# Performance work log

Measured on AMD Instinct MI355X. Metric: run time of the kernel, lower is better.

Reference implementation:

```python
import jax, jax.numpy as jnp
import numpy as np

B, P, K = 8, 1024, 20  # clouds, points per cloud, kNN neighbors
OUT = 40
EPS = 1e-5


def leaky(x):
    return jnp.where(x >= 0, x, 0.2 * x)


def batch_norm(h, gamma, beta):
    mu = jnp.mean(h, axis=0)
    var = jnp.var(h, axis=0)
    return (h - mu) * jax.lax.rsqrt(var + EPS) * gamma + beta


def edge_conv(x, W, b, k):
    # x: [B,P,C]. Dynamic kNN in feature space (self included, as torch_cluster knn),
    # edge feature nn([x_i, x_j - x_i]) (single plain Linear per PyG MLP plain_last),
    # then max-aggregation over the k neighbors.
    sq = jnp.sum(x * x, axis=-1)                                  # [B,P]
    d = sq[:, :, None] + sq[:, None, :] - 2.0 * jnp.einsum('bpc,bqc->bpq', x, x)
    idx = jax.lax.top_k(-d, k)[1]                                  # [B,P,k]
    xj = jax.vmap(lambda xc, ic: xc[ic])(x, idx)                   # [B,P,k,C]
    xi = jnp.broadcast_to(x[:, :, None, :], xj.shape)
    e = jnp.concatenate([xi, xj - xi], axis=-1)                    # [B,P,k,2C]
    h = jnp.einsum('bpke,ec->bpkc', e, W) + b
    return jnp.max(h, axis=2)                                      # [B,P,Cout]


def setup_inputs() -> dict:
    key = jax.random.key(0)
    ks = jax.random.split(key, 16)
    s = 0.1
    pos = jax.random.normal(ks[0], (B * P, 3), dtype=jnp.float32)
    batch = jnp.repeat(jnp.arange(B, dtype=jnp.int32), P)
    return {
        'pos': pos, 'batch': batch,
        'W1': jax.random.normal(ks[1], (6, 64), jnp.float32) * s,    'b1': jnp.zeros((64,), jnp.float32),
        'W2': jax.random.normal(ks[2], (128, 64), jnp.float32) * s,  'b2': jnp.zeros((64,), jnp.float32),
        'W3': jax.random.normal(ks[3], (128, 128), jnp.float32) * s, 'b3': jnp.zeros((128,), jnp.float32),
        'W4': jax.random.normal(ks[4], (256, 256), jnp.float32) * s, 'b4': jnp.zeros((256,), jnp.float32),
        'Wm': jax.random.normal(ks[5], (512, 1024), jnp.float32) * s, 'bm': jnp.zeros((1024,), jnp.float32),
        'Wa': jax.random.normal(ks[6], (2048, 512), jnp.float32) * s, 'ba': jnp.zeros((512,), jnp.float32),
        'ga': jnp.ones((512,), jnp.float32),  'bea': jnp.zeros((512,), jnp.float32),
        'Wb': jax.random.normal(ks[7], (512, 256), jnp.float32) * s, 'bb': jnp.zeros((256,), jnp.float32),
        'gb': jnp.ones((256,), jnp.float32),  'beb': jnp.zeros((256,), jnp.float32),
        'Wc': jax.random.normal(ks[8], (256, OUT), jnp.float32) * s, 'bc': jnp.zeros((OUT,), jnp.float32),
    }


def reference(pos, batch, W1, b1, W2, b2, W3, b3, W4, b4, Wm, bm,
              Wa, ba, ga, bea, Wb, bb, gb, beb, Wc, bc):
    # batch ids are contiguous with P points per cloud -> reshape to [B,P,.]
    x = pos.reshape(B, P, 3)
    x1 = edge_conv(x, W1, b1, K)    # [B,P,64]
    x2 = edge_conv(x1, W2, b2, K)   # [B,P,64]
    x3 = edge_conv(x2, W3, b3, K)   # [B,P,128]
    x4 = edge_conv(x3, W4, b4, K)   # [B,P,256]
    cat = jnp.concatenate([x1, x2, x3, x4], axis=-1)  # [B,P,512]
    out = cat @ Wm + bm                                # [B,P,1024] (plain Linear)
    gmax = jnp.max(out, axis=1)                        # global_max_pool  [B,1024]
    gmean = jnp.mean(out, axis=1)                      # global_mean_pool [B,1024]
    h = jnp.concatenate([gmax, gmean], axis=-1)        # [B,2048]
    h = leaky(batch_norm(h @ Wa + ba, ga, bea))        # dropout = identity (eval)
    h = leaky(batch_norm(h @ Wb + bb, gb, beb))
    return h @ Wc + bc                                 # [B,40]
```

## Files before the change

kernel.cpp:

```cpp
#include <hip/hip_runtime.h>
#include <hip/hip_bf16.h>

#define NB 8
#define NP 1024
#define NPTS (NB * NP)
#define KNN 20

using bf16x8 = __attribute__((ext_vector_type(8))) short;
using f32x4 = __attribute__((ext_vector_type(4))) float;
using u64x16 = __attribute__((ext_vector_type(16))) unsigned long long;
using u32x16 = __attribute__((ext_vector_type(16))) unsigned int;

static __device__ __forceinline__ unsigned long long umin64(unsigned long long a,
                                                            unsigned long long b) {
    return a < b ? a : b;
}

static __device__ __forceinline__ void split_bf16(float v, unsigned short& h,
                                                  unsigned short& l) {
    __hip_bfloat16 hb = __float2bfloat16(v);
    float hf = __bfloat162float(hb);
    __hip_bfloat16 lb = __float2bfloat16(v - hf);
    h = *(unsigned short*)&hb;
    l = *(unsigned short*)&lb;
}

static __device__ __forceinline__ unsigned long long wave_bitonic_sort(
        unsigned long long v, int lane) {
#pragma unroll
    for (int k = 2; k <= 64; k <<= 1) {
#pragma unroll
        for (int j = k >> 1; j > 0; j >>= 1) {
            unsigned long long o = __shfl_xor(v, j, 64);
            bool tmin = (((lane & k) == 0) == ((lane & j) == 0));
            bool lt = v < o;
            v = (lt == tmin) ? v : o;
        }
    }
    return v;
}

static __device__ __forceinline__ unsigned wave_bitonic_sort_u32(unsigned v, int lane) {
#pragma unroll
    for (int k = 2; k <= 64; k <<= 1) {
#pragma unroll
        for (int j = k >> 1; j > 0; j >>= 1) {
            unsigned o = (unsigned)__shfl_xor((int)v, j, 64);
            bool tmin = (((lane & k) == 0) == ((lane & j) == 0));
            bool lt = v < o;
            v = (lt == tmin) ? v : o;
        }
    }
    return v;
}

static __device__ __forceinline__ void topk20_wave(u64x16 k, int lane,
                                                   int* __restrict__ out) {
    for (int r = 0; r < KNN; ++r) {
        unsigned long long m = k[0];
#pragma unroll
        for (int j = 1; j < 16; ++j)
            if ((unsigned)(k[j] >> 32) < (unsigned)(m >> 32)) m = k[j];
#pragma unroll
        for (int s = 1; s < 64; s <<= 1) {
            unsigned long long o = __shfl_xor(m, s, 64);
            m = umin64(m, o);
        }
        if (lane == 0) out[r] = (int)(m & 0xffffffffu);
        if (r == KNN - 1) break;
        unsigned mlo = (unsigned)m;
#pragma unroll
        for (int j = 0; j < 16; ++j)
            if ((unsigned)k[j] == mlo) k[j] = ~0ull;
    }
}

static __device__ __forceinline__ void topk20_sel(u32x16 d, int lane,
                                                  unsigned long long* __restrict__ cand,
                                                  int* __restrict__ out) {
    unsigned lm = d[0];
#pragma unroll
    for (int j = 1; j < 16; ++j) lm = (d[j] < lm) ? d[j] : lm;
    unsigned srt = wave_bitonic_sort_u32(lm, lane);
    unsigned T = (unsigned)__shfl((int)srt, 19, 64);

    const unsigned long long below = (1ull << lane) - 1ull;
    int base = 0;
#pragma unroll
    for (int j = 0; j < 16; ++j) {
        bool sel = (d[j] <= T);
        unsigned long long mask = __ballot(sel);
        if (sel) {
            int pos = base + (int)__popcll(mask & below);
            if (pos < 64)
                cand[pos] = ((unsigned long long)d[j] << 32) | (unsigned)(j * 64 + lane);
        }
        base += (int)__popcll(mask);
    }

    if (base <= 64) {
        unsigned long long v = (lane < base) ? cand[lane] : ~0ull;
        unsigned hi = (unsigned)(v >> 32);
        unsigned hs = wave_bitonic_sort_u32(hi, lane);
        unsigned t2 = (unsigned)__shfl((int)hs, 19, 64);
        bool sel2 = (lane < base) && (hi <= t2);
        unsigned long long m2 = __ballot(sel2);
        if ((int)__popcll(m2) == KNN) {
            if (sel2) out[(int)__popcll(m2 & below)] = (int)(v & 0xffffffffu);
        } else {
            unsigned long long sv = wave_bitonic_sort(v, lane);
            if (lane < KNN) out[lane] = (int)(sv & 0xffffffffu);
        }
    } else {
        u64x16 k;
#pragma unroll
        for (int j = 0; j < 16; ++j)
            k[j] = ((unsigned long long)d[j] << 32) | (unsigned)(j * 64 + lane);
        topk20_wave(k, lane, out);
    }
}

struct Knn3Shared {
    float sx[3][1024];
    float ssq[1024];
    unsigned long long cand[4][64];
};
struct Edge1Shared {
    float sX[3][68];
    float sW[3][132];
};
union L1Shared {
    Knn3Shared k;
    Edge1Shared e;
};

struct KnnShared {
    float sD[16][1028];
    float sqa[16];
    float sqb[1024];
    unsigned long long cand[4][64];
};
struct EdgeShared {
    uint4 sAh[2][4][132];
    uint4 sAl[2][4][132];
    uint4 sBh[2][4][132];
    uint4 sBl[2][4][132];
};
union LayerShared {
    KnnShared k;
    EdgeShared e;
};

__global__ __launch_bounds__(256) void knn3_edge_kernel(const float* __restrict__ x,
                                                        const float* __restrict__ W,
                                                        const float* __restrict__ bias,
                                                        int* __restrict__ idx,
                                                        float* __restrict__ AB) {
    __shared__ L1Shared su;
    const int bid = blockIdx.x;
    const int tid = threadIdx.x;

    if (bid < 512) {
        Knn3Shared& S = su.k;
        const int wid = tid >> 6, lane = tid & 63;
        const int b = bid >> 6, p0 = (bid & 63) * 16;
        const int g0 = b * NP;
        const float* xb = x + (size_t)g0 * 3;

        for (int t = tid; t < 1024; t += 256) {
            float vx = xb[t * 3 + 0], vy = xb[t * 3 + 1], vz = xb[t * 3 + 2];
            S.sx[0][t] = vx;
            S.sx[1][t] = vy;
            S.sx[2][t] = vz;
            S.ssq[t] = vx * vx + vy * vy + vz * vz;
        }
        __syncthreads();

        for (int rr = 0; rr < 4; ++rr) {
            int pr = p0 + wid * 4 + rr;
            const float px = S.sx[0][pr], py = S.sx[1][pr], pz = S.sx[2][pr];
            const float sqp = S.ssq[pr];
            u32x16 d;
#pragma unroll
            for (int j = 0; j < 16; ++j) {
                int q = j * 64 + lane;
                float dot = px * S.sx[0][q];
                dot += py * S.sx[1][q];
                dot += pz * S.sx[2][q];
                float dv = sqp + S.ssq[q] - 2.0f * dot;
                unsigned u = __float_as_uint(dv);
                d[j] = (u & 0x80000000u) ? ~u : (u | 0x80000000u);
            }
            topk20_sel(d, lane, S.cand[wid], idx + (size_t)(g0 + pr) * KNN);
        }
    } else {
        Edge1Shared& S = su.e;
        constexpr int Cin = 3, Cout = 64, N2 = 128;
        const int p0 = (bid - 512) * 64;
        const int tx = tid & 15, ty = tid >> 4;

        for (int t = tid; t < 64 * Cin; t += 256) {
            int m = t / Cin, c = t - m * Cin;
            S.sX[c][m] = x[(size_t)(p0 + m) * Cin + c];
        }
        for (int t = tid; t < Cin * 128; t += 256) {
            int c = t >> 7, n = t & 127;
            float w;
            if (n < Cout)
                w = W[(size_t)c * Cout + n] - W[(size_t)(Cin + c) * Cout + n];
            else
                w = W[(size_t)(Cin + c) * Cout + (n - Cout)];
            S.sW[c][n] = w;
        }
        __syncthreads();

        float acc[4][8];
#pragma unroll
        for (int i = 0; i < 4; ++i)
#pragma unroll
            for (int j = 0; j < 8; ++j) acc[i][j] = 0.f;

#pragma unroll
        for (int c = 0; c < Cin; ++c) {
            float4 a4 = *(const float4*)&S.sX[c][ty * 4];
            float4 w0 = *(const float4*)&S.sW[c][tx * 4];
            float4 w1 = *(const float4*)&S.sW[c][64 + tx * 4];
            float av[4] = {a4.x, a4.y, a4.z, a4.w};
#pragma unroll
            for (int i = 0; i < 4; ++i) {
                acc[i][0] += av[i] * w0.x;
                acc[i][1] += av[i] * w0.y;
                acc[i][2] += av[i] * w0.z;
                acc[i][3] += av[i] * w0.w;
                acc[i][4] += av[i] * w1.x;
                acc[i][5] += av[i] * w1.y;
                acc[i][6] += av[i] * w1.z;
                acc[i][7] += av[i] * w1.w;
            }
        }

        float4 bb0 = *(const float4*)&bias[tx * 4];
#pragma unroll
        for (int i = 0; i < 4; ++i) {
            float* orow = AB + (size_t)(p0 + ty * 4 + i) * N2;
            float4 o0, o1;
            o0.x = acc[i][0] + bb0.x;
            o0.y = acc[i][1] + bb0.y;
            o0.z = acc[i][2] + bb0.z;
            o0.w = acc[i][3] + bb0.w;
            o1.x = acc[i][4];
            o1.y = acc[i][5];
            o1.z = acc[i][6];
            o1.w = acc[i][7];
            *(float4*)&orow[tx * 4] = o0;
            *(float4*)&orow[64 + tx * 4] = o1;
        }
    }
}

template <int C, int Cout>
__global__ __launch_bounds__(256, 2) void layer_kernel(
        const unsigned short* __restrict__ Xhp, const unsigned short* __restrict__ Xlp,
        const float* __restrict__ sqn, int* __restrict__ idx,
        const unsigned short* __restrict__ Whp, const unsigned short* __restrict__ Wlp,
        const float* __restrict__ bias, float* __restrict__ AB) {
    __shared__ LayerShared su;
    constexpr int NCK = C / 32;
    const int bid = blockIdx.x;
    const int tid = threadIdx.x;
    const int wid = tid >> 6, lane = tid & 63;
    const int fkb = lane >> 4, flm = lane & 15;
    const uint4* Ah4 = (const uint4*)Xhp;
    const uint4* Al4 = (const uint4*)Xlp;

    if (bid < 512) {
        KnnShared& S = su.k;
        const int b = bid >> 6, rg = bid & 63;
        const int g0 = b * NP;
        const int p0 = rg * 16;

        if (tid < 16) S.sqa[tid] = sqn[g0 + p0 + tid];
        for (int t = tid; t < 1024; t += 256) S.sqb[t] = sqn[g0 + t];
        __syncthreads();

        uint4 fAh[NCK], fAl[NCK];
#pragma unroll
        for (int kk = 0; kk < NCK; ++kk) {
            size_t a = (size_t)(4 * kk + fkb) * NPTS + g0 + p0 + flm;
            fAh[kk] = Ah4[a];
            fAl[kk] = Al4[a];
        }

        const int r4 = fkb * 4, cc = flm;

#pragma unroll
        for (int t = 0; t < 2; ++t) {
            const int c0 = (wid + t * 4) * 128;
            f32x4 acc[8];
#pragma unroll
            for (int j = 0; j < 8; ++j) acc[j] = {0.f, 0.f, 0.f, 0.f};

#pragma unroll
            for (int kk = 0; kk < NCK; ++kk) {
                uint4 fBh[8], fBl[8];
#pragma unroll
                for (int j = 0; j < 8; ++j) {
                    size_t bi = (size_t)(4 * kk + fkb) * NPTS + g0 + c0 + j * 16 + flm;
                    fBh[j] = Ah4[bi];
                    fBl[j] = Al4[bi];
                }
                bf16x8 ah = *(const bf16x8*)&fAh[kk];
                bf16x8 al = *(const bf16x8*)&fAl[kk];
#pragma unroll
                for (int j = 0; j < 8; ++j) {
                    bf16x8 bh = *(const bf16x8*)&fBh[j];
                    bf16x8 bl = *(const bf16x8*)&fBl[j];
                    acc[j] = __builtin_amdgcn_mfma_f32_16x16x32_bf16(ah, bh, acc[j], 0, 0, 0);
                    acc[j] = __builtin_amdgcn_mfma_f32_16x16x32_bf16(ah, bl, acc[j], 0, 0, 0);
                    acc[j] = __builtin_amdgcn_mfma_f32_16x16x32_bf16(al, bh, acc[j], 0, 0, 0);
                }
            }

#pragma unroll
            for (int r = 0; r < 4; ++r) {
                int row = r4 + r;
                float sp = S.sqa[row];
#pragma unroll
                for (int j = 0; j < 8; ++j) {
                    int col = c0 + j * 16 + cc;
                    S.sD[row][col] = sp + S.sqb[col] - 2.0f * acc[j][r];
                }
            }
        }
        __syncthreads();

        for (int rr = 0; rr < 4; ++rr) {
            int row = wid * 4 + rr;
            u32x16 d;
#pragma unroll
            for (int j = 0; j < 16; ++j) {
                int q = j * 64 + lane;
                unsigned u = __float_as_uint(S.sD[row][q]);
                d[j] = (u & 0x80000000u) ? ~u : (u | 0x80000000u);
            }
            topk20_sel(d, lane, S.cand[wid], idx + (size_t)(g0 + p0 + row) * KNN);
        }
    } else {
        EdgeShared& S = su.e;
        constexpr int N2 = 2 * Cout;
        constexpr int NX = N2 / 128;
        const int eb = bid - 512;
        const int n0 = (eb % NX) * 128;
        const int p0 = (eb / NX) * 128;
        const int wm = (wid >> 1) * 64, wn = (wid & 1) * 64;

        f32x4 acc[4][4];
#pragma unroll
        for (int i = 0; i < 4; ++i)
#pragma unroll
            for (int j = 0; j < 4; ++j) acc[i][j] = {0.f, 0.f, 0.f, 0.f};

        const uint4* Wh4 = (const uint4*)Whp;
        const uint4* Wl4 = (const uint4*)Wlp;

        const int m0 = tid & 127, kb0 = tid >> 7;
        uint4 rAh0, rAl0, rBh0, rBl0, rAh1, rAl1, rBh1, rBl1;

#define EM_LOAD(ck)                                                     \
    {                                                                   \
        int ksb = (ck) * 4;                                             \
        size_t a0 = (size_t)(ksb + kb0) * NPTS + p0 + m0;               \
        size_t a1 = (size_t)(ksb + kb0 + 2) * NPTS + p0 + m0;           \
        size_t b0 = (size_t)(ksb + kb0) * N2 + n0 + m0;                 \
        size_t b1 = (size_t)(ksb + kb0 + 2) * N2 + n0 + m0;             \
        rAh0 = Ah4[a0]; rAl0 = Al4[a0];                                 \
        rAh1 = Ah4[a1]; rAl1 = Al4[a1];                                 \
        rBh0 = Wh4[b0]; rBl0 = Wl4[b0];                                 \
        rBh1 = Wh4[b1]; rBl1 = Wl4[b1];                                 \
    }

#define EM_WRITE(buf)                                                         \
    {                                                                         \
        S.sAh[buf][kb0][m0] = rAh0;  S.sAl[buf][kb0][m0] = rAl0;              \
        S.sAh[buf][kb0 + 2][m0] = rAh1;  S.sAl[buf][kb0 + 2][m0] = rAl1;      \
        S.sBh[buf][kb0][m0] = rBh0;  S.sBl[buf][kb0][m0] = rBl0;              \
        S.sBh[buf][kb0 + 2][m0] = rBh1;  S.sBl[buf][kb0 + 2][m0] = rBl1;      \
    }

        EM_LOAD(0);
        EM_WRITE(0);
        __syncthreads();

        for (int ck = 0; ck < NCK; ++ck) {
            const int buf = ck & 1;
            if (ck < NCK - 1) EM_LOAD(ck + 1);

            bf16x8 fAh[4], fAl[4], fBh[4], fBl[4];
#pragma unroll
            for (int i = 0; i < 4; ++i) {
                fAh[i] = *(const bf16x8*)&S.sAh[buf][fkb][wm + i * 16 + flm];
                fAl[i] = *(const bf16x8*)&S.sAl[buf][fkb][wm + i * 16 + flm];
                fBh[i] = *(const bf16x8*)&S.sBh[buf][fkb][wn + i * 16 + flm];
                fBl[i] = *(const bf16x8*)&S.sBl[buf][fkb][wn + i * 16 + flm];
            }
#pragma unroll
            for (int i = 0; i < 4; ++i)
#pragma unroll
                for (int j = 0; j < 4; ++j) {
                    acc[i][j] = __builtin_amdgcn_mfma_f32_16x16x32_bf16(
                            fAh[i], fBh[j], acc[i][j], 0, 0, 0);
                    acc[i][j] = __builtin_amdgcn_mfma_f32_16x16x32_bf16(
                            fAh[i], fBl[j], acc[i][j], 0, 0, 0);
                    acc[i][j] = __builtin_amdgcn_mfma_f32_16x16x32_bf16(
                            fAl[i], fBh[j], acc[i][j], 0, 0, 0);
                }

            if (ck < NCK - 1) EM_WRITE(buf ^ 1);
            __syncthreads();
        }

        const int r4 = (lane >> 4) * 4, cc = lane & 15;
        float bj[4];
#pragma unroll
        for (int j = 0; j < 4; ++j) {
            int cg = n0 + wn + j * 16 + cc;
            bj[j] = (cg < Cout) ? bias[cg] : 0.f;
        }
#pragma unroll
        for (int i = 0; i < 4; ++i) {
#pragma unroll
            for (int r = 0; r < 4; ++r) {
                int row = wm + i * 16 + r4 + r;
                float* orow = AB + (size_t)(p0 + row) * N2 + n0;
#pragma unroll
                for (int j = 0; j < 4; ++j)
                    orow[wn + j * 16 + cc] = acc[i][j][r] + bj[j];
            }
        }
#undef EM_LOAD
#undef EM_WRITE
    }
}

template <int Cout, bool WSQ>
__global__ __launch_bounds__(256) void gather_max_panel_kernel(
        const float* __restrict__ AB, const int* __restrict__ idx,
        float* __restrict__ y, unsigned short* __restrict__ Xh,
        unsigned short* __restrict__ Xl, float* __restrict__ sqn) {
    constexpr int N2 = 2 * Cout;
    constexpr int TPP = Cout / 4;
    constexpr int PPB = 256 / TPP;
    constexpr int RS = N2 / 4;
    const int pp = threadIdx.x / TPP;
    const int t = threadIdx.x % TPP;
    const int p = blockIdx.x * PPB + pp;
    const int base = p & ~(NP - 1);

    __shared__ int s_idx[PPB][KNN];
    __shared__ float srow[PPB][Cout];
    for (int tt = threadIdx.x; tt < PPB * KNN; tt += 256) {
        int a = tt / KNN, r = tt - a * KNN;
        s_idx[a][r] = idx[(size_t)(blockIdx.x * PPB + a) * KNN + r];
    }
    __syncthreads();

    const float4* Brow = (const float4*)(AB + (size_t)base * N2 + Cout);

    int q0 = s_idx[pp][0];
    float4 m = Brow[(size_t)q0 * RS + t];
#pragma unroll
    for (int j = 1; j < KNN; ++j) {
        int q = s_idx[pp][j];
        float4 v = Brow[(size_t)q * RS + t];
        m.x = fmaxf(m.x, v.x);
        m.y = fmaxf(m.y, v.y);
        m.z = fmaxf(m.z, v.z);
        m.w = fmaxf(m.w, v.w);
    }
    float4 a = *(const float4*)(AB + (size_t)p * N2 + 4 * t);
    float4 o;
    o.x = a.x + m.x;
    o.y = a.y + m.y;
    o.z = a.z + m.z;
    o.w = a.w + m.w;
    *(float4*)(y + (size_t)p * Cout + 4 * t) = o;

    unsigned short h[4], l[4];
    split_bf16(o.x, h[0], l[0]);
    split_bf16(o.y, h[1], l[1]);
    split_bf16(o.z, h[2], l[2]);
    split_bf16(o.w, h[3], l[3]);
    const int ks = t >> 1;
    size_t u2 = ((size_t)ks * NPTS + p) * 2 + (t & 1);
    uint2 hp, lp;
    hp.x = h[0] | ((unsigned)h[1] << 16);
    hp.y = h[2] | ((unsigned)h[3] << 16);
    lp.x = l[0] | ((unsigned)l[1] << 16);
    lp.y = l[2] | ((unsigned)l[3] << 16);
    ((uint2*)Xh)[u2] = hp;
    ((uint2*)Xl)[u2] = lp;

    if constexpr (WSQ) {
        *(float4*)&srow[pp][4 * t] = o;
        __syncthreads();
        if (t == 0) {
            float s = 0.f;
            for (int c = 0; c < Cout; ++c) {
                float v = srow[pp][c];
                s += v * v;
            }
            sqn[p] = s;
        }
    }
}

static __device__ __forceinline__ void pack_store(unsigned short h[8],
                                                  unsigned short l[8], size_t ci,
                                                  unsigned short* __restrict__ Wh,
                                                  unsigned short* __restrict__ Wl) {
    uint4 hp, lp;
    hp.x = h[0] | ((unsigned)h[1] << 16);
    hp.y = h[2] | ((unsigned)h[3] << 16);
    hp.z = h[4] | ((unsigned)h[5] << 16);
    hp.w = h[6] | ((unsigned)h[7] << 16);
    lp.x = l[0] | ((unsigned)l[1] << 16);
    lp.y = l[2] | ((unsigned)l[3] << 16);
    lp.z = l[4] | ((unsigned)l[5] << 16);
    lp.w = l[6] | ((unsigned)l[7] << 16);
    ((uint4*)Wh)[ci] = hp;
    ((uint4*)Wl)[ci] = lp;
}

static __device__ void conv_edge_w(const float* __restrict__ W, int Cin, int Cout,
                                   int g, unsigned short* __restrict__ Wh,
                                   unsigned short* __restrict__ Wl) {
    int N2 = 2 * Cout;
    if (g >= (Cin / 8) * N2) return;
    int n = g % N2, ks = g / N2;
    unsigned short h[8], l[8];
#pragma unroll
    for (int j = 0; j < 8; ++j) {
        int c = ks * 8 + j;
        float v;
        if (n < Cout)
            v = W[(size_t)c * Cout + n] - W[(size_t)(Cin + c) * Cout + n];
        else
            v = W[(size_t)(Cin + c) * Cout + (n - Cout)];
        split_bf16(v, h[j], l[j]);
    }
    pack_store(h, l, (size_t)ks * N2 + n, Wh, Wl);
}

__global__ __launch_bounds__(256) void convert_all_w_kernel(
        const float* __restrict__ Wm, const float* __restrict__ W2,
        const float* __restrict__ W3, const float* __restrict__ W4,
        unsigned short* __restrict__ Wmh, unsigned short* __restrict__ Wml,
        unsigned short* __restrict__ W2h, unsigned short* __restrict__ W2l,
        unsigned short* __restrict__ W3h, unsigned short* __restrict__ W3l,
        unsigned short* __restrict__ W4h, unsigned short* __restrict__ W4l) {
    int bid = blockIdx.x;
    if (bid < 256) {
        int g = bid * 256 + threadIdx.x;
        int n = g & 1023, ks = g >> 10;
        unsigned short h[8], l[8];
#pragma unroll
        for (int j = 0; j < 8; ++j) {
            float v = Wm[(size_t)(ks * 8 + j) * 1024 + n];
            split_bf16(v, h[j], l[j]);
        }
        pack_store(h, l, (size_t)ks * 1024 + n, Wmh, Wml);
    } else if (bid < 288) {
        conv_edge_w(W4, 128, 256, (bid - 256) * 256 + threadIdx.x, W4h, W4l);
    } else if (bid < 296) {
        conv_edge_w(W3, 64, 128, (bid - 288) * 256 + threadIdx.x, W3h, W3l);
    } else {
        conv_edge_w(W2, 64, 64, (bid - 296) * 256 + threadIdx.x, W2h, W2l);
    }
}

__global__ __launch_bounds__(256) void catmean_kernel(
        const float* __restrict__ x1, const float* __restrict__ x2,
        const float* __restrict__ x3, const float* __restrict__ x4,
        float* __restrict__ catmean) {
    const int n0 = blockIdx.x * 128;
    const int b = blockIdx.y;
    const int tid = threadIdx.x;
    const int col = n0 + (tid & 127);
    const int half = tid >> 7;
    __shared__ float sred[256];

    const float* src;
    int cw, coff;
    if (col < 64) { src = x1; cw = 64; coff = col; }
    else if (col < 128) { src = x2; cw = 64; coff = col - 64; }
    else if (col < 256) { src = x3; cw = 128; coff = col - 128; }
    else { src = x4; cw = 256; coff = col - 256; }

    float s = 0.f;
    const float* base = src + ((size_t)b * NP + half * 512) * cw + coff;
    for (int p = 0; p < 512; ++p) s += base[(size_t)p * cw];
    sred[tid] = s;
    __syncthreads();
    if (tid < 128)
        catmean[(size_t)b * 512 + col] = (sred[tid] + sred[tid + 128]) * (1.0f / 1024.0f);
}

__global__ __launch_bounds__(256) void gmean_kernel(const float* __restrict__ catmean,
                                                    const float* __restrict__ Wm,
                                                    const float* __restrict__ bm,
                                                    float* __restrict__ gmeanv) {
    const int n0 = blockIdx.x * 128;
    const int b = blockIdx.y;
    const int tid = threadIdx.x;
    const int cg = tid & 31, kp = tid >> 5;
    const int col = n0 + cg * 4;
    __shared__ float4 part[8][32];

    float4 acc = {0.f, 0.f, 0.f, 0.f};
    for (int k = kp * 64; k < kp * 64 + 64; ++k) {
        float g = catmean[(size_t)b * 512 + k];
        float4 w = *(const float4*)&Wm[(size_t)k * 1024 + col];
        acc.x += g * w.x;
        acc.y += g * w.y;
        acc.z += g * w.z;
        acc.w += g * w.w;
    }
    part[kp][cg] = acc;
    __syncthreads();
    if (tid < 32) {
        float4 s = part[0][tid];
#pragma unroll
        for (int z = 1; z < 8; ++z) {
            float4 p = part[z][tid];
            s.x += p.x; s.y += p.y; s.z += p.z; s.w += p.w;
        }
        float4 bb = *(const float4*)&bm[n0 + tid * 4];
        s.x += bb.x; s.y += bb.y; s.z += bb.z; s.w += bb.w;
        *(float4*)&gmeanv[(size_t)b * 1024 + n0 + tid * 4] = s;
    }
}

__global__ __launch_bounds__(256, 2) void gemm_cat_pool_kernel(
        const unsigned short* __restrict__ Ahp, const unsigned short* __restrict__ Alp,
        const unsigned short* __restrict__ Whp, const unsigned short* __restrict__ Wlp,
        float* __restrict__ pmax) {
    const int bid = blockIdx.x;
    const int xcd = bid & 7, pos = bid >> 3;
    const int nb = pos & 7, pb = (xcd << 3) | (pos >> 3);
    const int n0 = nb * 128, p0 = pb * 128;
    const int tid = threadIdx.x;
    const int wid = tid >> 6, lane = tid & 63;
    const int wm = (wid >> 1) * 64, wn = (wid & 1) * 64;

    __shared__ uint4 sAh[2][4][132], sAl[2][4][132], sBh[2][4][132], sBl[2][4][132];
    __shared__ float sMax[2][128];

    f32x4 acc[4][4];
#pragma unroll
    for (int i = 0; i < 4; ++i)
#pragma unroll
        for (int j = 0; j < 4; ++j) acc[i][j] = {0.f, 0.f, 0.f, 0.f};

    const uint4* Ah4 = (const uint4*)Ahp;
    const uint4* Al4 = (const uint4*)Alp;
    const uint4* Wh4 = (const uint4*)Whp;
    const uint4* Wl4 = (const uint4*)Wlp;

    const int m0 = tid & 127, kb0 = tid >> 7;
    uint4 rAh0, rAl0, rBh0, rBl0, rAh1, rAl1, rBh1, rBl1;

#define MP_LOAD(ck)                                                     \
    {                                                                   \
        int ksb = (ck) * 4;                                             \
        size_t a0 = (size_t)(ksb + kb0) * 8192 + p0 + m0;               \
        size_t a1 = (size_t)(ksb + kb0 + 2) * 8192 + p0 + m0;           \
        size_t b0 = (size_t)(ksb + kb0) * 1024 + n0 + m0;               \
        size_t b1 = (size_t)(ksb + kb0 + 2) * 1024 + n0 + m0;           \
        rAh0 = Ah4[a0]; rAl0 = Al4[a0];                                 \
        rAh1 = Ah4[a1]; rAl1 = Al4[a1];                                 \
        rBh0 = Wh4[b0]; rBl0 = Wl4[b0];                                 \
        rBh1 = Wh4[b1]; rBl1 = Wl4[b1];                                 \
    }

#define MP_WRITE(buf)                                                   \
    {                                                                   \
        sAh[buf][kb0][m0] = rAh0;  sAl[buf][kb0][m0] = rAl0;            \
        sAh[buf][kb0 + 2][m0] = rAh1;  sAl[buf][kb0 + 2][m0] = rAl1;    \
        sBh[buf][kb0][m0] = rBh0;  sBl[buf][kb0][m0] = rBl0;            \
        sBh[buf][kb0 + 2][m0] = rBh1;  sBl[buf][kb0 + 2][m0] = rBl1;    \
    }

    MP_LOAD(0);
    MP_WRITE(0);
    __syncthreads();

    const int fkb = lane >> 4, flm = lane & 15;

    for (int ck = 0; ck < 16; ++ck) {
        const int buf = ck & 1;
        if (ck < 15) MP_LOAD(ck + 1);

        bf16x8 fAh[4], fAl[4], fBh[4], fBl[4];
#pragma unroll
        for (int i = 0; i < 4; ++i) {
            fAh[i] = *(const bf16x8*)&sAh[buf][fkb][wm + i * 16 + flm];
            fAl[i] = *(const bf16x8*)&sAl[buf][fkb][wm + i * 16 + flm];
            fBh[i] = *(const bf16x8*)&sBh[buf][fkb][wn + i * 16 + flm];
            fBl[i] = *(const bf16x8*)&sBl[buf][fkb][wn + i * 16 + flm];
        }
#pragma unroll
        for (int i = 0; i < 4; ++i)
#pragma unroll
            for (int j = 0; j < 4; ++j) {
                acc[i][j] = __builtin_amdgcn_mfma_f32_16x16x32_bf16(fAh[i], fBh[j],
                                                                    acc[i][j], 0, 0, 0);
                acc[i][j] = __builtin_amdgcn_mfma_f32_16x16x32_bf16(fAh[i], fBl[j],
                                                                    acc[i][j], 0, 0, 0);
                acc[i][j] = __builtin_amdgcn_mfma_f32_16x16x32_bf16(fAl[i], fBh[j],
                                                                    acc[i][j], 0, 0, 0);
            }

        if (ck < 15) MP_WRITE(buf ^ 1);
        __syncthreads();
    }

    float cm[4];
#pragma unroll
    for (int j = 0; j < 4; ++j) {
        float m = acc[0][j][0];
#pragma unroll
        for (int i = 0; i < 4; ++i)
#pragma unroll
            for (int r = 0; r < 4; ++r) m = fmaxf(m, acc[i][j][r]);
        m = fmaxf(m, __shfl_xor(m, 16, 64));
        m = fmaxf(m, __shfl_xor(m, 32, 64));
        cm[j] = m;
    }
    if (lane < 16) {
#pragma unroll
        for (int j = 0; j < 4; ++j) sMax[wid >> 1][wn + j * 16 + lane] = cm[j];
    }
    __syncthreads();
    if (tid < 128)
        pmax[(size_t)pb * 1024 + n0 + tid] = fmaxf(sMax[0][tid], sMax[1][tid]);
#undef MP_LOAD
#undef MP_WRITE
}

__global__ __launch_bounds__(256) void fc_a_kernel(const float* __restrict__ pmax,
                                                   const float* __restrict__ gmeanv,
                                                   const float* __restrict__ bm,
                                                   const float* __restrict__ Wa,
                                                   const float* __restrict__ ba,
                                                   float* __restrict__ ha) {
    const int b = blockIdx.y;
    const int n0 = blockIdx.x * 64;
    const int tid = threadIdx.x;
    __shared__ float gm[2048];
    __shared__ float4 part[16][16];

    for (int c = tid; c < 1024; c += 256) {
        float m = pmax[(size_t)(b * 8) * 1024 + c];
#pragma unroll
        for (int z = 1; z < 8; ++z) m = fmaxf(m, pmax[(size_t)(b * 8 + z) * 1024 + c]);
        gm[c] = m + bm[c];
        gm[1024 + c] = gmeanv[(size_t)b * 1024 + c];
    }
    __syncthreads();

    const int cg = tid & 15, kp = tid >> 4;
    const int co = n0 + cg * 4;
    float4 acc = {0.f, 0.f, 0.f, 0.f};
    const float* Wp = Wa + (size_t)(kp * 128) * 512 + co;
    const float* gp = gm + kp * 128;
#pragma unroll 8
    for (int k = 0; k < 128; ++k) {
        float g = gp[k];
        float4 w = *(const float4*)&Wp[(size_t)k * 512];
        acc.x += g * w.x;
        acc.y += g * w.y;
        acc.z += g * w.z;
        acc.w += g * w.w;
    }
    part[kp][cg] = acc;
    __syncthreads();
    if (tid < 16) {
        float4 s = part[0][tid];
#pragma unroll
        for (int z = 1; z < 16; ++z) {
            float4 p = part[z][tid];
            s.x += p.x; s.y += p.y; s.z += p.z; s.w += p.w;
        }
        float4 bb = *(const float4*)&ba[n0 + tid * 4];
        s.x += bb.x; s.y += bb.y; s.z += bb.z; s.w += bb.w;
        *(float4*)&ha[(size_t)b * 512 + n0 + tid * 4] = s;
    }
}

__global__ __launch_bounds__(256) void fc_b_bn_kernel(const float* __restrict__ ha,
                                                      const float* __restrict__ g,
                                                      const float* __restrict__ be,
                                                      const float* __restrict__ Wb,
                                                      const float* __restrict__ bb,
                                                      float* __restrict__ hb) {
    const int b = blockIdx.y;
    const int n0 = blockIdx.x * 64;
    const int tid = threadIdx.x;
    __shared__ float shall[NB][512];
    __shared__ float sh[512];
    __shared__ float4 part[16][16];

    for (int t = tid; t < NB * 512; t += 256) shall[t >> 9][t & 511] = ha[t];
    __syncthreads();

    for (int c = tid; c < 512; c += 256) {
        float mu = 0.f;
        for (int z = 0; z < NB; ++z) mu += shall[z][c];
        mu *= 0.125f;
        float var = 0.f;
        for (int z = 0; z < NB; ++z) {
            float d = shall[z][c] - mu;
            var += d * d;
        }
        var *= 0.125f;
        float inv = 1.0f / sqrtf(var + 1e-5f);
        float v = (shall[b][c] - mu) * inv * g[c] + be[c];
        sh[c] = v >= 0.f ? v : 0.2f * v;
    }
    __syncthreads();

    const int cg = tid & 15, kp = tid >> 4;
    const int co = n0 + cg * 4;
    float4 acc = {0.f, 0.f, 0.f, 0.f};
#pragma unroll 8
    for (int k = 0; k < 32; ++k) {
        float gg = sh[kp * 32 + k];
        float4 w = *(const float4*)&Wb[(size_t)(kp * 32 + k) * 256 + co];
        acc.x += gg * w.x;
        acc.y += gg * w.y;
        acc.z += gg * w.z;
        acc.w += gg * w.w;
    }
    part[kp][cg] = acc;
    __syncthreads();
    if (tid < 16) {
        float4 s = part[0][tid];
#pragma unroll
        for (int z = 1; z < 16; ++z) {
            float4 p = part[z][tid];
            s.x += p.x; s.y += p.y; s.z += p.z; s.w += p.w;
        }
        float4 bv = *(const float4*)&bb[n0 + tid * 4];
        s.x += bv.x; s.y += bv.y; s.z += bv.z; s.w += bv.w;
        *(float4*)&hb[(size_t)b * 256 + n0 + tid * 4] = s;
    }
}

__global__ __launch_bounds__(256) void fc_c_bn_kernel(const float* __restrict__ hbin,
                                                      const float* __restrict__ g,
                                                      const float* __restrict__ be,
                                                      const float* __restrict__ Wc,
                                                      const float* __restrict__ bc,
                                                      float* __restrict__ outp) {
    const int tid = threadIdx.x;
    __shared__ float shn[NB][256];

    {
        int c = tid;
        float col[NB];
#pragma unroll
        for (int z = 0; z < NB; ++z) col[z] = hbin[z * 256 + c];
        float mu = 0.f;
#pragma unroll
        for (int z = 0; z < NB; ++z) mu += col[z];
        mu *= 0.125f;
        float var = 0.f;
#pragma unroll
        for (int z = 0; z < NB; ++z) {
            float d = col[z] - mu;
            var += d * d;
        }
        var *= 0.125f;
        float inv = 1.0f / sqrtf(var + 1e-5f);
#pragma unroll
        for (int z = 0; z < NB; ++z) {
            float v = (col[z] - mu) * inv * g[c] + be[c];
            shn[z][c] = v >= 0.f ? v : 0.2f * v;
        }
    }
    __syncthreads();

    int t = blockIdx.x * 256 + tid;
    if (t < 8 * 40) {
        int b = t / 40, o = t - b * 40;
        float s = bc[o];
        for (int c = 0; c < 256; ++c) s += shn[b][c] * Wc[c * 40 + o];
        outp[t] = s;
    }
}

extern "C" void kernel_launch(void* const* d_in, const int* in_sizes, int n_in,
                              void* d_out, int out_size, void* d_ws, size_t ws_size,
                              hipStream_t stream) {
    const float* pos = (const float*)d_in[0];
    const float* W1 = (const float*)d_in[2];
    const float* b1 = (const float*)d_in[3];
    const float* W2 = (const float*)d_in[4];
    const float* b2 = (const float*)d_in[5];
    const float* W3 = (const float*)d_in[6];
    const float* b3 = (const float*)d_in[7];
    const float* W4 = (const float*)d_in[8];
    const float* b4 = (const float*)d_in[9];
    const float* Wm = (const float*)d_in[10];
    const float* bm = (const float*)d_in[11];
    const float* Wa = (const float*)d_in[12];
    const float* ba = (const float*)d_in[13];
    const float* ga = (const float*)d_in[14];
    const float* bea = (const float*)d_in[15];
    const float* Wb = (const float*)d_in[16];
    const float* bb = (const float*)d_in[17];
    const float* gb = (const float*)d_in[18];
    const float* beb = (const float*)d_in[19];
    const float* Wc = (const float*)d_in[20];
    const float* bc = (const float*)d_in[21];
    float* out = (float*)d_out;

    char* ws = (char*)d_ws;
    size_t off = 0;
    auto alloc = [&](size_t bytes) {
        void* p = ws + off;
        off += (bytes + 255) & ~(size_t)255;
        return p;
    };
    int* idx = (int*)alloc((size_t)NPTS * KNN * 4);
    float* x1 = (float*)alloc((size_t)NPTS * 64 * 4);
    float* x2 = (float*)alloc((size_t)NPTS * 64 * 4);
    float* x3 = (float*)alloc((size_t)NPTS * 128 * 4);
    float* x4 = (float*)alloc((size_t)NPTS * 256 * 4);
    float* scratch = (float*)alloc((size_t)NPTS * 512 * 4);
    float* pmax = (float*)alloc((size_t)64 * 1024 * 4);
    float* catmean = (float*)alloc(NB * 512 * 4);
    float* gmeanv = (float*)alloc(NB * 1024 * 4);
    float* ha = (float*)alloc(NB * 512 * 4);
    float* hb = (float*)alloc(NB * 256 * 4);
    float* sqn = (float*)alloc(NPTS * 4);
    unsigned short* Ach = (unsigned short*)alloc((size_t)64 * NPTS * 8 * 2);
    unsigned short* Acl = (unsigned short*)alloc((size_t)64 * NPTS * 8 * 2);
    unsigned short* Wth = (unsigned short*)alloc((size_t)64 * 1024 * 8 * 2);
    unsigned short* Wtl = (unsigned short*)alloc((size_t)64 * 1024 * 8 * 2);
    unsigned short* W2h = (unsigned short*)alloc((size_t)8 * 128 * 8 * 2);
    unsigned short* W2l = (unsigned short*)alloc((size_t)8 * 128 * 8 * 2);
    unsigned short* W3h = (unsigned short*)alloc((size_t)8 * 256 * 8 * 2);
    unsigned short* W3l = (unsigned short*)alloc((size_t)8 * 256 * 8 * 2);
    unsigned short* W4h = (unsigned short*)alloc((size_t)16 * 512 * 8 * 2);
    unsigned short* W4l = (unsigned short*)alloc((size_t)16 * 512 * 8 * 2);
    (void)ws_size;

    float* AB = scratch;
    const size_t REG = (size_t)NPTS * 8;
    unsigned short* x1h = Ach, *x1l = Acl;
    unsigned short* x2h = Ach + 8 * REG, *x2l = Acl + 8 * REG;
    unsigned short* x3h = Ach + 16 * REG, *x3l = Acl + 16 * REG;
    unsigned short* x4h = Ach + 32 * REG, *x4l = Acl + 32 * REG;

    convert_all_w_kernel<<<300, 256, 0, stream>>>(Wm, W2, W3, W4, Wth, Wtl, W2h, W2l,
                                                  W3h, W3l, W4h, W4l);

    knn3_edge_kernel<<<640, 256, 0, stream>>>(pos, W1, b1, idx, AB);
    gather_max_panel_kernel<64, true><<<NPTS / 16, 256, 0, stream>>>(AB, idx, x1, x1h,
                                                                     x1l, sqn);

    layer_kernel<64, 64><<<512 + 64, 256, 0, stream>>>(x1h, x1l, sqn, idx, W2h, W2l,
                                                       b2, AB);
    gather_max_panel_kernel<64, true><<<NPTS / 16, 256, 0, stream>>>(AB, idx, x2, x2h,
                                                                     x2l, sqn);

    layer_kernel<64, 128><<<512 + 128, 256, 0, stream>>>(x2h, x2l, sqn, idx, W3h, W3l,
                                                         b3, AB);
    gather_max_panel_kernel<128, true><<<NPTS / 8, 256, 0, stream>>>(AB, idx, x3, x3h,
                                                                     x3l, sqn);

    layer_kernel<128, 256><<<512 + 256, 256, 0, stream>>>(x3h, x3l, sqn, idx, W4h, W4l,
                                                          b4, AB);
    gather_max_panel_kernel<256, false><<<NPTS / 4, 256, 0, stream>>>(AB, idx, x4, x4h,
                                                                      x4l, nullptr);

    catmean_kernel<<<dim3(4, NB), 256, 0, stream>>>(x1, x2, x3, x4, catmean);
    gmean_kernel<<<dim3(8, NB), 256, 0, stream>>>(catmean, Wm, bm, gmeanv);

    gemm_cat_pool_kernel<<<512, 256, 0, stream>>>(Ach, Acl, Wth, Wtl, pmax);

    fc_a_kernel<<<dim3(8, NB), 256, 0, stream>>>(pmax, gmeanv, bm, Wa, ba, ha);
    fc_b_bn_kernel<<<dim3(4, NB), 256, 0, stream>>>(ha, ga, bea, Wb, bb, hb);
    fc_c_bn_kernel<<<2, 256, 0, stream>>>(hb, gb, beb, Wc, bc, out);
}
```

Baseline: 222.2 us.

## Merge weight conversion into first kNN kernel and fuse mean-pool path into pooled GEMM

```diff
diff --git a/kernel.cpp b/kernel.cpp
--- a/kernel.cpp
+++ b/kernel.cpp
@@ -118,6 +118,43 @@
             k[j] = ((unsigned long long)d[j] << 32) | (unsigned)(j * 64 + lane);
         topk20_wave(k, lane, out);
     }
+}
+
+static __device__ __forceinline__ void pack_store(unsigned short h[8],
+                                                  unsigned short l[8], size_t ci,
+                                                  unsigned short* __restrict__ Wh,
+                                                  unsigned short* __restrict__ Wl) {
+    uint4 hp, lp;
+    hp.x = h[0] | ((unsigned)h[1] << 16);
+    hp.y = h[2] | ((unsigned)h[3] << 16);
+    hp.z = h[4] | ((unsigned)h[5] << 16);
+    hp.w = h[6] | ((unsigned)h[7] << 16);
+    lp.x = l[0] | ((unsigned)l[1] << 16);
+    lp.y = l[2] | ((unsigned)l[3] << 16);
+    lp.z = l[4] | ((unsigned)l[5] << 16);
+    lp.w = l[6] | ((unsigned)l[7] << 16);
+    ((uint4*)Wh)[ci] = hp;
+    ((uint4*)Wl)[ci] = lp;
+}
+
+static __device__ void conv_edge_w(const float* __restrict__ W, int Cin, int Cout,
+                                   int g, unsigned short* __restrict__ Wh,
+                                   unsigned short* __restrict__ Wl) {
+    int N2 = 2 * Cout;
+    if (g >= (Cin / 8) * N2) return;
+    int n = g % N2, ks = g / N2;
+    unsigned short h[8], l[8];
+#pragma unroll
+    for (int j = 0; j < 8; ++j) {
+        int c = ks * 8 + j;
+        float v;
+        if (n < Cout)
+            v = W[(size_t)c * Cout + n] - W[(size_t)(Cin + c) * Cout + n];
+        else
+            v = W[(size_t)(Cin + c) * Cout + (n - Cout)];
+        split_bf16(v, h[j], l[j]);
+    }
+    pack_store(h, l, (size_t)ks * N2 + n, Wh, Wl);
 }
 
 struct Knn3Shared {
@@ -151,11 +188,32 @@
     EdgeShared e;
 };
 
-__global__ __launch_bounds__(256) void knn3_edge_kernel(const float* __restrict__ x,
-                                                        const float* __restrict__ W,
-                                                        const float* __restrict__ bias,
-                                                        int* __restrict__ idx,
-                                                        float* __restrict__ AB) {
+struct PoolShared {
+    uint4 sAh[2][4][132];
+    uint4 sAl[2][4][132];
+    uint4 sBh[2][4][132];
+    uint4 sBl[2][4][132];
+    float sMax[2][128];
+};
+struct CmGmShared {
+    float sred[256];
+    float scm[512];
+    float4 part[8][32];
+};
+union PoolUnion {
+    PoolShared p;
+    CmGmShared c;
+};
+
+__global__ __launch_bounds__(256) void knn3_edge_conv_kernel(
+        const float* __restrict__ x, const float* __restrict__ W,
+        const float* __restrict__ bias, int* __restrict__ idx, float* __restrict__ AB,
+        const float* __restrict__ Wm, const float* __restrict__ W2,
+        const float* __restrict__ W3, const float* __restrict__ W4,
+        unsigned short* __restrict__ Wmh, unsigned short* __restrict__ Wml,
+        unsigned short* __restrict__ W2h, unsigned short* __restrict__ W2l,
+        unsigned short* __restrict__ W3h, unsigned short* __restrict__ W3l,
+        unsigned short* __restrict__ W4h, unsigned short* __restrict__ W4l) {
     __shared__ L1Shared su;
     const int bid = blockIdx.x;
     const int tid = threadIdx.x;
@@ -193,7 +251,7 @@
             }
             topk20_sel(d, lane, S.cand[wid], idx + (size_t)(g0 + pr) * KNN);
         }
-    } else {
+    } else if (bid < 640) {
         Edge1Shared& S = su.e;
         constexpr int Cin = 3, Cout = 64, N2 = 128;
         const int p0 = (bid - 512) * 64;
@@ -254,6 +312,25 @@
             o1.w = acc[i][7];
             *(float4*)&orow[tx * 4] = o0;
             *(float4*)&orow[64 + tx * 4] = o1;
+        }
+    } else {
+        int cid = bid - 640;
+        if (cid < 256) {
+            int g = cid * 256 + tid;
+            int n = g & 1023, ks = g >> 10;
+            unsigned short h[8], l[8];
+#pragma unroll
+            for (int j = 0; j < 8; ++j) {
+                float v = Wm[(size_t)(ks * 8 + j) * 1024 + n];
+                split_bf16(v, h[j], l[j]);
+            }
+            pack_store(h, l, (size_t)ks * 1024 + n, Wmh, Wml);
+        } else if (cid < 288) {
+            conv_edge_w(W4, 128, 256, (cid - 256) * 256 + tid, W4h, W4l);
+        } else if (cid < 296) {
+            conv_edge_w(W3, 64, 128, (cid - 288) * 256 + tid, W3h, W3l);
+        } else {
+            conv_edge_w(W2, 64, 64, (cid - 296) * 256 + tid, W2h, W2l);
         }
     }
 }
@@ -514,160 +591,38 @@
     }
 }
 
-static __device__ __forceinline__ void pack_store(unsigned short h[8],
-                                                  unsigned short l[8], size_t ci,
-                                                  unsigned short* __restrict__ Wh,
-                                                  unsigned short* __restrict__ Wl) {
-    uint4 hp, lp;
-    hp.x = h[0] | ((unsigned)h[1] << 16);
-    hp.y = h[2] | ((unsigned)h[3] << 16);
-    hp.z = h[4] | ((unsigned)h[5] << 16);
-    hp.w = h[6] | ((unsigned)h[7] << 16);
-    lp.x = l[0] | ((unsigned)l[1] << 16);
-    lp.y = l[2] | ((unsigned)l[3] << 16);
-    lp.z = l[4] | ((unsigned)l[5] << 16);
-    lp.w = l[6] | ((unsigned)l[7] << 16);
-    ((uint4*)Wh)[ci] = hp;
-    ((uint4*)Wl)[ci] = lp;
-}
-
-static __device__ void conv_edge_w(const float* __restrict__ W, int Cin, int Cout,
-                                   int g, unsigned short* __restrict__ Wh,
-                                   unsigned short* __restrict__ Wl) {
-    int N2 = 2 * Cout;
-    if (g >= (Cin / 8) * N2) return;
-    int n = g % N2, ks = g / N2;
-    unsigned short h[8], l[8];
-#pragma unroll
-    for (int j = 0; j < 8; ++j) {
-        int c = ks * 8 + j;
-        float v;
-        if (n < Cout)
-            v = W[(size_t)c * Cout + n] - W[(size_t)(Cin + c) * Cout + n];
-        else
-            v = W[(size_t)(Cin + c) * Cout + (n - Cout)];
-        split_bf16(v, h[j], l[j]);
-    }
-    pack_store(h, l, (size_t)ks * N2 + n, Wh, Wl);
-}
-
-__global__ __launch_bounds__(256) void convert_all_w_kernel(
-        const float* __restrict__ Wm, const float* __restrict__ W2,
-        const float* __restrict__ W3, const float* __restrict__ W4,
-        unsigned short* __restrict__ Wmh, unsigned short* __restrict__ Wml,
-        unsigned short* __restrict__ W2h, unsigned short* __restrict__ W2l,
-        unsigned short* __restrict__ W3h, unsigned short* __restrict__ W3l,
-        unsigned short* __restrict__ W4h, unsigned short* __restrict__ W4l) {
-    int bid = blockIdx.x;
-    if (bid < 256) {
-        int g = bid * 256 + threadIdx.x;
-        int n = g & 1023, ks = g >> 10;
-        unsigned short h[8], l[8];
-#pragma unroll
-        for (int j = 0; j < 8; ++j) {
-            float v = Wm[(size_t)(ks * 8 + j) * 1024 + n];
-            split_bf16(v, h[j], l[j]);
-        }
-        pack_store(h, l, (size_t)ks * 1024 + n, Wmh, Wml);
-    } else if (bid < 288) {
-        conv_edge_w(W4, 128, 256, (bid - 256) * 256 + threadIdx.x, W4h, W4l);
-    } else if (bid < 296) {
-        conv_edge_w(W3, 64, 128, (bid - 288) * 256 + threadIdx.x, W3h, W3l);
-    } else {
-        conv_edge_w(W2, 64, 64, (bid - 296) * 256 + threadIdx.x, W2h, W2l);
-    }
-}
-
-__global__ __launch_bounds__(256) void catmean_kernel(
-        const float* __restrict__ x1, const float* __restrict__ x2,
-        const float* __restrict__ x3, const float* __restrict__ x4,
-        float* __restrict__ catmean) {
-    const int n0 = blockIdx.x * 128;
-    const int b = blockIdx.y;
-    const int tid = threadIdx.x;
-    const int col = n0 + (tid & 127);
-    const int half = tid >> 7;
-    __shared__ float sred[256];
-
-    const float* src;
-    int cw, coff;
-    if (col < 64) { src = x1; cw = 64; coff = col; }
-    else if (col < 128) { src = x2; cw = 64; coff = col - 64; }
-    else if (col < 256) { src = x3; cw = 128; coff = col - 128; }
-    else { src = x4; cw = 256; coff = col - 256; }
-
-    float s = 0.f;
-    const float* base = src + ((size_t)b * NP + half * 512) * cw + coff;
-    for (int p = 0; p < 512; ++p) s += base[(size_t)p * cw];
-    sred[tid] = s;
-    __syncthreads();
-    if (tid < 128)
-        catmean[(size_t)b * 512 + col] = (sred[tid] + sred[tid + 128]) * (1.0f / 1024.0f);
-}
-
-__global__ __launch_bounds__(256) void gmean_kernel(const float* __restrict__ catmean,
-                                                    const float* __restrict__ Wm,
-                                                    const float* __restrict__ bm,
-                                                    float* __restrict__ gmeanv) {
-    const int n0 = blockIdx.x * 128;
-    const int b = blockIdx.y;
-    const int tid = threadIdx.x;
-    const int cg = tid & 31, kp = tid >> 5;
-    const int col = n0 + cg * 4;
-    __shared__ float4 part[8][32];
-
-    float4 acc = {0.f, 0.f, 0.f, 0.f};
-    for (int k = kp * 64; k < kp * 64 + 64; ++k) {
-        float g = catmean[(size_t)b * 512 + k];
-        float4 w = *(const float4*)&Wm[(size_t)k * 1024 + col];
-        acc.x += g * w.x;
-        acc.y += g * w.y;
-        acc.z += g * w.z;
-        acc.w += g * w.w;
-    }
-    part[kp][cg] = acc;
-    __syncthreads();
-    if (tid < 32) {
-        float4 s = part[0][tid];
-#pragma unroll
-        for (int z = 1; z < 8; ++z) {
-            float4 p = part[z][tid];
-            s.x += p.x; s.y += p.y; s.z += p.z; s.w += p.w;
-        }
-        float4 bb = *(const float4*)&bm[n0 + tid * 4];
-        s.x += bb.x; s.y += bb.y; s.z += bb.z; s.w += bb.w;
-        *(float4*)&gmeanv[(size_t)b * 1024 + n0 + tid * 4] = s;
-    }
-}
-
-__global__ __launch_bounds__(256, 2) void gemm_cat_pool_kernel(
+__global__ __launch_bounds__(256, 2) void gemm_cat_pool_cm_kernel(
         const unsigned short* __restrict__ Ahp, const unsigned short* __restrict__ Alp,
         const unsigned short* __restrict__ Whp, const unsigned short* __restrict__ Wlp,
-        float* __restrict__ pmax) {
+        float* __restrict__ pmax, const float* __restrict__ x1,
+        const float* __restrict__ x2, const float* __restrict__ x3,
+        const float* __restrict__ x4, const float* __restrict__ Wm,
+        const float* __restrict__ bm, float* __restrict__ gmeanv) {
+    __shared__ PoolUnion su;
     const int bid = blockIdx.x;
-    const int xcd = bid & 7, pos = bid >> 3;
-    const int nb = pos & 7, pb = (xcd << 3) | (pos >> 3);
-    const int n0 = nb * 128, p0 = pb * 128;
     const int tid = threadIdx.x;
-    const int wid = tid >> 6, lane = tid & 63;
-    const int wm = (wid >> 1) * 64, wn = (wid & 1) * 64;
-
-    __shared__ uint4 sAh[2][4][132], sAl[2][4][132], sBh[2][4][132], sBl[2][4][132];
-    __shared__ float sMax[2][128];
-
-    f32x4 acc[4][4];
-#pragma unroll
-    for (int i = 0; i < 4; ++i)
-#pragma unroll
-        for (int j = 0; j < 4; ++j) acc[i][j] = {0.f, 0.f, 0.f, 0.f};
-
-    const uint4* Ah4 = (const uint4*)Ahp;
-    const uint4* Al4 = (const uint4*)Alp;
-    const uint4* Wh4 = (const uint4*)Whp;
-    const uint4* Wl4 = (const uint4*)Wlp;
-
-    const int m0 = tid & 127, kb0 = tid >> 7;
-    uint4 rAh0, rAl0, rBh0, rBl0, rAh1, rAl1, rBh1, rBl1;
+
+    if (bid < 512) {
+        PoolShared& S = su.p;
+        const int xcd = bid & 7, pos = bid >> 3;
+        const int nb = pos & 7, pb = (xcd << 3) | (pos >> 3);
+        const int n0 = nb * 128, p0 = pb * 128;
+        const int wid = tid >> 6, lane = tid & 63;
+        const int wm = (wid >> 1) * 64, wn = (wid & 1) * 64;
+
+        f32x4 acc[4][4];
+#pragma unroll
+        for (int i = 0; i < 4; ++i)
+#pragma unroll
+            for (int j = 0; j < 4; ++j) acc[i][j] = {0.f, 0.f, 0.f, 0.f};
+
+        const uint4* Ah4 = (const uint4*)Ahp;
+        const uint4* Al4 = (const uint4*)Alp;
+        const uint4* Wh4 = (const uint4*)Whp;
+        const uint4* Wl4 = (const uint4*)Wlp;
+
+        const int m0 = tid & 127, kb0 = tid >> 7;
+        uint4 rAh0, rAl0, rBh0, rBl0, rAh1, rAl1, rBh1, rBl1;
 
 #define MP_LOAD(ck)                                                     \
     {                                                                   \
@@ -682,69 +637,121 @@
         rBh1 = Wh4[b1]; rBl1 = Wl4[b1];                                 \
     }
 
-#define MP_WRITE(buf)                                                   \
-    {                                                                   \
-        sAh[buf][kb0][m0] = rAh0;  sAl[buf][kb0][m0] = rAl0;            \
-        sAh[buf][kb0 + 2][m0] = rAh1;  sAl[buf][kb0 + 2][m0] = rAl1;    \
-        sBh[buf][kb0][m0] = rBh0;  sBl[buf][kb0][m0] = rBl0;            \
-        sBh[buf][kb0 + 2][m0] = rBh1;  sBl[buf][kb0 + 2][m0] = rBl1;    \
-    }
-
-    MP_LOAD(0);
-    MP_WRITE(0);
-    __syncthreads();
-
-    const int fkb = lane >> 4, flm = lane & 15;
-
-    for (int ck = 0; ck < 16; ++ck) {
-        const int buf = ck & 1;
-        if (ck < 15) MP_LOAD(ck + 1);
-
-        bf16x8 fAh[4], fAl[4], fBh[4], fBl[4];
-#pragma unroll
-        for (int i = 0; i < 4; ++i) {
-            fAh[i] = *(const bf16x8*)&sAh[buf][fkb][wm + i * 16 + flm];
-            fAl[i] = *(const bf16x8*)&sAl[buf][fkb][wm + i * 16 + flm];
-            fBh[i] = *(const bf16x8*)&sBh[buf][fkb][wn + i * 16 + flm];
-            fBl[i] = *(const bf16x8*)&sBl[buf][fkb][wn + i * 16 + flm];
-        }
-#pragma unroll
-        for (int i = 0; i < 4; ++i)
-#pragma unroll
-            for (int j = 0; j < 4; ++j) {
-                acc[i][j] = __builtin_amdgcn_mfma_f32_16x16x32_bf16(fAh[i], fBh[j],
-                                                                    acc[i][j], 0, 0, 0);
-                acc[i][j] = __builtin_amdgcn_mfma_f32_16x16x32_bf16(fAh[i], fBl[j],
-                                                                    acc[i][j], 0, 0, 0);
-                acc[i][j] = __builtin_amdgcn_mfma_f32_16x16x32_bf16(fAl[i], fBh[j],
-                                                                    acc[i][j], 0, 0, 0);
-            }
-
-        if (ck < 15) MP_WRITE(buf ^ 1);
+#define MP_WRITE(buf)                                                         \
+    {                                                                         \
+        S.sAh[buf][kb0][m0] = rAh0;  S.sAl[buf][kb0][m0] = rAl0;              \
+        S.sAh[buf][kb0 + 2][m0] = rAh1;  S.sAl[buf][kb0 + 2][m0] = rAl1;      \
+        S.sBh[buf][kb0][m0] = rBh0;  S.sBl[buf][kb0][m0] = rBl0;              \
+        S.sBh[buf][kb0 + 2][m0] = rBh1;  S.sBl[buf][kb0 + 2][m0] = rBl1;      \
+    }
+
+        MP_LOAD(0);
+        MP_WRITE(0);
         __syncthreads();
-    }
-
-    float cm[4];
-#pragma unroll
-    for (int j = 0; j < 4; ++j) {
-        float m = acc[0][j][0];
-#pragma unroll
-        for (int i = 0; i < 4; ++i)
-#pragma unroll
-            for (int r = 0; r < 4; ++r) m = fmaxf(m, acc[i][j][r]);
-        m = fmaxf(m, __shfl_xor(m, 16, 64));
-        m = fmaxf(m, __shfl_xor(m, 32, 64));
-        cm[j] = m;
-    }
-    if (lane < 16) {
-#pragma unroll
-        for (int j = 0; j < 4; ++j) sMax[wid >> 1][wn + j * 16 + lane] = cm[j];
-    }
-    __syncthreads();
-    if (tid < 128)
-        pmax[(size_t)pb * 1024 + n0 + tid] = fmaxf(sMax[0][tid], sMax[1][tid]);
+
+        const int fkb = lane >> 4, flm = lane & 15;
+
+        for (int ck = 0; ck < 16; ++ck) {
+            const int buf = ck & 1;
+            if (ck < 15) MP_LOAD(ck + 1);
+
+            bf16x8 fAh[4], fAl[4], fBh[4], fBl[4];
+#pragma unroll
+            for (int i = 0; i < 4; ++i) {
+                fAh[i] = *(const bf16x8*)&S.sAh[buf][fkb][wm + i * 16 + flm];
+                fAl[i] = *(const bf16x8*)&S.sAl[buf][fkb][wm + i * 16 + flm];
+                fBh[i] = *(const bf16x8*)&S.sBh[buf][fkb][wn + i * 16 + flm];
+                fBl[i] = *(const bf16x8*)&S.sBl[buf][fkb][wn + i * 16 + flm];
+            }
+#pragma unroll
+            for (int i = 0; i < 4; ++i)
+#pragma unroll
+                for (int j = 0; j < 4; ++j) {
+                    acc[i][j] = __builtin_amdgcn_mfma_f32_16x16x32_bf16(
+                            fAh[i], fBh[j], acc[i][j], 0, 0, 0);
+                    acc[i][j] = __builtin_amdgcn_mfma_f32_16x16x32_bf16(
+                            fAh[i], fBl[j], acc[i][j], 0, 0, 0);
+                    acc[i][j] = __builtin_amdgcn_mfma_f32_16x16x32_bf16(
+                            fAl[i], fBh[j], acc[i][j], 0, 0, 0);
+                }
+
+            if (ck < 15) MP_WRITE(buf ^ 1);
+            __syncthreads();
+        }
+
+        float cm[4];
+#pragma unroll
+        for (int j = 0; j < 4; ++j) {
+            float m = acc[0][j][0];
+#pragma unroll
+            for (int i = 0; i < 4; ++i)
+#pragma unroll
+                for (int r = 0; r < 4; ++r) m = fmaxf(m, acc[i][j][r]);
+            m = fmaxf(m, __shfl_xor(m, 16, 64));
+            m = fmaxf(m, __shfl_xor(m, 32, 64));
+            cm[j] = m;
+        }
+        if (lane < 16) {
+#pragma unroll
+            for (int j = 0; j < 4; ++j) S.sMax[wid >> 1][wn + j * 16 + lane] = cm[j];
+        }
+        __syncthreads();
+        if (tid < 128)
+            pmax[(size_t)pb * 1024 + n0 + tid] = fmaxf(S.sMax[0][tid], S.sMax[1][tid]);
 #undef MP_LOAD
 #undef MP_WRITE
+    } else {
+        CmGmShared& S = su.c;
+        const int b = bid - 512;
+
+        for (int n0 = 0; n0 < 512; n0 += 128) {
+            const int col = n0 + (tid & 127);
+            const int half = tid >> 7;
+            const float* src;
+            int cw, coff;
+            if (col < 64) { src = x1; cw = 64; coff = col; }
+            else if (col < 128) { src = x2; cw = 64; coff = col - 64; }
+            else if (col < 256) { src = x3; cw = 128; coff = col - 128; }
+            else { src = x4; cw = 256; coff = col - 256; }
+
+            float s = 0.f;
+            const float* base = src + ((size_t)b * NP + half * 512) * cw + coff;
+            for (int p = 0; p < 512; ++p) s += base[(size_t)p * cw];
+            S.sred[tid] = s;
+            __syncthreads();
+            if (tid < 128)
+                S.scm[n0 + tid] = (S.sred[tid] + S.sred[tid + 128]) * (1.0f / 1024.0f);
+            __syncthreads();
+        }
+
+        for (int n0 = 0; n0 < 1024; n0 += 128) {
+            const int cg = tid & 31, kp = tid >> 5;
+            const int col = n0 + cg * 4;
+            float4 acc = {0.f, 0.f, 0.f, 0.f};
+            for (int k = kp * 64; k < kp * 64 + 64; ++k) {
+                float g = S.scm[k];
+                float4 w = *(const float4*)&Wm[(size_t)k * 1024 + col];
+                acc.x += g * w.x;
+                acc.y += g * w.y;
+                acc.z += g * w.z;
+                acc.w += g * w.w;
+            }
+            S.part[kp][cg] = acc;
+            __syncthreads();
+            if (tid < 32) {
+                float4 s = S.part[0][tid];
+#pragma unroll
+                for (int z = 1; z < 8; ++z) {
+                    float4 p = S.part[z][tid];
+                    s.x += p.x; s.y += p.y; s.z += p.z; s.w += p.w;
+                }
+                float4 bb = *(const float4*)&bm[n0 + tid * 4];
+                s.x += bb.x; s.y += bb.y; s.z += bb.z; s.w += bb.w;
+                *(float4*)&gmeanv[(size_t)b * 1024 + n0 + tid * 4] = s;
+            }
+            __syncthreads();
+        }
+    }
 }
 
 __global__ __launch_bounds__(256) void fc_a_kernel(const float* __restrict__ pmax,
@@ -939,7 +946,6 @@
     float* x4 = (float*)alloc((size_t)NPTS * 256 * 4);
     float* scratch = (float*)alloc((size_t)NPTS * 512 * 4);
     float* pmax = (float*)alloc((size_t)64 * 1024 * 4);
-    float* catmean = (float*)alloc(NB * 512 * 4);
     float* gmeanv = (float*)alloc(NB * 1024 * 4);
     float* ha = (float*)alloc(NB * 512 * 4);
     float* hb = (float*)alloc(NB * 256 * 4);
@@ -963,10 +969,9 @@
     unsigned short* x3h = Ach + 16 * REG, *x3l = Acl + 16 * REG;
     unsigned short* x4h = Ach + 32 * REG, *x4l = Acl + 32 * REG;
 
-    convert_all_w_kernel<<<300, 256, 0, stream>>>(Wm, W2, W3, W4, Wth, Wtl, W2h, W2l,
-                                                  W3h, W3l, W4h, W4l);
-
-    knn3_edge_kernel<<<640, 256, 0, stream>>>(pos, W1, b1, idx, AB);
+    knn3_edge_conv_kernel<<<940, 256, 0, stream>>>(pos, W1, b1, idx, AB, Wm, W2, W3,
+                                                   W4, Wth, Wtl, W2h, W2l, W3h, W3l,
+                                                   W4h, W4l);
     gather_max_panel_kernel<64, true><<<NPTS / 16, 256, 0, stream>>>(AB, idx, x1, x1h,
                                                                      x1l, sqn);
 
@@ -985,10 +990,8 @@
     gather_max_panel_kernel<256, false><<<NPTS / 4, 256, 0, stream>>>(AB, idx, x4, x4h,
                                                                       x4l, nullptr);
 
-    catmean_kernel<<<dim3(4, NB), 256, 0, stream>>>(x1, x2, x3, x4, catmean);
-    gmean_kernel<<<dim3(8, NB), 256, 0, stream>>>(catmean, Wm, bm, gmeanv);
-
-    gemm_cat_pool_kernel<<<512, 256, 0, stream>>>(Ach, Acl, Wth, Wtl, pmax);
+    gemm_cat_pool_cm_kernel<<<520, 256, 0, stream>>>(Ach, Acl, Wth, Wtl, pmax, x1, x2,
+                                                     x3, x4, Wm, bm, gmeanv);
 
     fc_a_kernel<<<dim3(8, NB), 256, 0, stream>>>(pmax, gmeanv, bm, Wa, ba, ha);
     fc_b_bn_kernel<<<dim3(4, NB), 256, 0, stream>>>(ha, ga, bea, Wb, bb, hb);
```

New measurement: 255.7 us. +15.1%, slower.
